# Kernel optimization log

Measured on AMD Instinct MI355X. Metric: run time of the kernel, lower is better.

The kernel has to match this reference:

```python
import math
import jax, jax.numpy as jnp
import numpy as np

B, L, H, E = 16, 2048, 8, 64
FACTOR = 1


def setup_inputs() -> dict:
    key = jax.random.key(0)
    kq, kk, kv = jax.random.split(key, 3)
    queries = jax.random.normal(kq, (B, L, H, E), dtype=jnp.float32)
    keys = jax.random.normal(kk, (B, L, H, E), dtype=jnp.float32)
    values = jax.random.normal(kv, (B, L, H, E), dtype=jnp.float32)
    return {"queries": queries, "keys": keys, "values": values, "attn_mask": 0}


def reference(queries, keys, values, attn_mask):
    # queries/keys/values: [B, L, H, E]; attn_mask is unused (as in the original).
    b, l, h, e = queries.shape
    # [B, H, E, L]
    qp = jnp.transpose(queries, (0, 2, 3, 1))
    kp = jnp.transpose(keys, (0, 2, 3, 1))
    vp = jnp.transpose(values, (0, 2, 3, 1))

    # Period-based dependency discovery via FFT cross-correlation.
    qf = jnp.fft.rfft(qp, axis=-1)
    kf = jnp.fft.rfft(kp, axis=-1)
    corr = jnp.fft.irfft(qf * jnp.conj(kf), n=l, axis=-1)  # [B, H, E, L]

    # Inference-style time-delay aggregation (per-batch top-k delays).
    top_k = max(1, int(FACTOR * math.log(l)))
    mean_value = corr.mean(axis=(1, 2))  # [B, L]
    weights, delay = jax.lax.top_k(mean_value, top_k)  # [B, K]
    tmp_corr = jax.nn.softmax(weights, axis=-1)  # [B, K]

    # Gather from doubled tensor == circular roll: index (t + delay) mod L.
    idx = (jnp.arange(l)[None, None, :] + delay[:, :, None]) % l  # [B, K, L]
    # vp[:, None]: [B, 1, H, E, L]; idx broadcast to [B, K, 1, 1, L]
    pattern = jnp.take_along_axis(vp[:, None], idx[:, :, None, None, :], axis=-1)  # [B, K, H, E, L]
    agg = jnp.einsum('bkhel,bk->bhel', pattern, tmp_corr)  # [B, H, E, L]

    return jnp.transpose(agg, (0, 3, 1, 2))  # [B, L, H, E]
```

## Files before the change

### kernel.cpp

```cpp
#include <hip/hip_runtime.h>
#include <hip/hip_fp16.h>
#include <cstdint>
#include <cstddef>

#define BB 16
#define LL 2048
#define CC 512
#define TK 7
#define PDC(a) ((a) + ((a) >> 4))
#define PSTR 1056
#define NG 128

typedef float2 cf;
typedef __attribute__((ext_vector_type(4))) float f32x4v;

__device__ inline cf cadd(cf a, cf b){ return make_float2(a.x + b.x, a.y + b.y); }
__device__ inline cf csub(cf a, cf b){ return make_float2(a.x - b.x, a.y - b.y); }
__device__ inline cf cmul(cf a, cf b){ return make_float2(a.x*b.x - a.y*b.y, a.x*b.y + a.y*b.x); }

template<int S> __device__ inline cf crot(cf z){
  return (S < 0) ? make_float2(z.y, -z.x) : make_float2(-z.y, z.x);
}

template<int S> __device__ inline void dft4(cf* x){
  const cf t0 = cadd(x[0], x[2]), t1 = csub(x[0], x[2]);
  const cf t2 = cadd(x[1], x[3]), t3 = csub(x[1], x[3]);
  const cf r = crot<S>(t3);
  x[0] = cadd(t0, t2); x[2] = csub(t0, t2);
  x[1] = cadd(t1, r);  x[3] = csub(t1, r);
}

template<int S> __device__ inline void dft8(cf* x){
  cf e[4] = { x[0], x[2], x[4], x[6] };
  cf o[4] = { x[1], x[3], x[5], x[7] };
  dft4<S>(e); dft4<S>(o);
  const float H = 0.70710678118654752440f;
  o[1] = cmul(o[1], make_float2(H, (float)S * H));
  o[2] = crot<S>(o[2]);
  o[3] = cmul(o[3], make_float2(-H, (float)S * H));
  x[0] = cadd(e[0], o[0]); x[4] = csub(e[0], o[0]);
  x[1] = cadd(e[1], o[1]); x[5] = csub(e[1], o[1]);
  x[2] = cadd(e[2], o[2]); x[6] = csub(e[2], o[2]);
  x[3] = cadd(e[3], o[3]); x[7] = csub(e[3], o[3]);
}

struct Tw { cf w2[7], w3[7], w4a[3], w4b[3]; };

template<int S>
__device__ inline void make_tw(int tid, Tw& T){
  const float base = (float)S * 6.283185307179586f / 2048.0f;
  const int j7 = tid & 7, j63 = tid & 63;
#pragma unroll
  for (int i = 0; i < 7; ++i){
    float s, c;
    __sincosf(base * (float)(32 * (i + 1) * j7), &s, &c);  T.w2[i] = make_float2(c, s);
    __sincosf(base * (float)( 4 * (i + 1) * j63), &s, &c); T.w3[i] = make_float2(c, s);
  }
#pragma unroll
  for (int i = 0; i < 3; ++i){
    float s, c;
    __sincosf(base * (float)((i + 1) * tid), &s, &c);         T.w4a[i] = make_float2(c, s);
    __sincosf(base * (float)((i + 1) * (tid + 256)), &s, &c); T.w4b[i] = make_float2(c, s);
  }
}

template<int S>
__device__ inline void fft_s123(cf* Bc, cf* Cc, cf* x, const Tw& T, int tid){
  dft8<S>(x);
#pragma unroll
  for (int t = 0; t < 8; ++t) Bc[PDC((tid << 3) + t)] = x[t];
  __syncthreads();
  {
    cf y[8];
#pragma unroll
    for (int t = 0; t < 8; ++t) y[t] = Bc[PDC(tid + (t << 8))];
#pragma unroll
    for (int t = 1; t < 8; ++t) y[t] = cmul(y[t], T.w2[t - 1]);
    dft8<S>(y);
    const int base = ((tid >> 3) << 6) + (tid & 7);
#pragma unroll
    for (int t = 0; t < 8; ++t) Cc[PDC(base + (t << 3))] = y[t];
  }
  __syncthreads();
  {
    cf y[8];
#pragma unroll
    for (int t = 0; t < 8; ++t) y[t] = Cc[PDC(tid + (t << 8))];
#pragma unroll
    for (int t = 1; t < 8; ++t) y[t] = cmul(y[t], T.w3[t - 1]);
    dft8<S>(y);
    const int base = ((tid >> 6) << 9) + (tid & 63);
#pragma unroll
    for (int t = 0; t < 8; ++t) Bc[PDC(base + (t << 6))] = y[t];
  }
  __syncthreads();
}

__global__ __launch_bounds__(256) void transpose_pack(const float* __restrict__ q,
                                                      const float* __restrict__ k,
                                                      __half2* __restrict__ z){
  int bid = blockIdx.x;
  const int tt = bid & 31; bid >>= 5;
  const int ct = bid & 7;  bid >>= 3;
  const int b = bid;
  const int t0 = tt << 6, c0 = ct << 6;
  __shared__ __half2 T[64][69];
  const int tid = threadIdx.x;
  const size_t inbase = ((size_t)b * LL + t0) * CC + c0;
  const int c4 = (tid & 15) << 2;
  f32x4v a[4], e[4];
#pragma unroll
  for (int p2 = 0; p2 < 4; ++p2){
    const int row = (p2 << 4) + (tid >> 4);
    a[p2] = __builtin_nontemporal_load(
        reinterpret_cast<const f32x4v*>(q + inbase + (size_t)row * CC + c4));
    e[p2] = __builtin_nontemporal_load(
        reinterpret_cast<const f32x4v*>(k + inbase + (size_t)row * CC + c4));
  }
#pragma unroll
  for (int p2 = 0; p2 < 4; ++p2){
    const int row = (p2 << 4) + (tid >> 4);
    T[row][c4 + 0] = __floats2half2_rn(a[p2][0], e[p2][0]);
    T[row][c4 + 1] = __floats2half2_rn(a[p2][1], e[p2][1]);
    T[row][c4 + 2] = __floats2half2_rn(a[p2][2], e[p2][2]);
    T[row][c4 + 3] = __floats2half2_rn(a[p2][3], e[p2][3]);
  }
  __syncthreads();
  const size_t outbase = ((size_t)b * CC + c0) * LL + (size_t)t0;
#pragma unroll
  for (int it = 0; it < 4; ++it){
    const int idx = (it << 8) + tid;
    const int c = idx >> 4;
    const int t4 = (idx & 15) << 2;
    const __half2 u0 = T[t4 + 0][c], u1 = T[t4 + 1][c];
    const __half2 u2 = T[t4 + 2][c], u3 = T[t4 + 3][c];
    uint4 w;
    w.x = *reinterpret_cast<const uint*>(&u0);
    w.y = *reinterpret_cast<const uint*>(&u1);
    w.z = *reinterpret_cast<const uint*>(&u2);
    w.w = *reinterpret_cast<const uint*>(&u3);
    *reinterpret_cast<uint4*>(&z[outbase + (size_t)c * LL + t4]) = w;
  }
}

__global__ __launch_bounds__(256) void fft_fwd(const __half2* __restrict__ z,
                                               float2* __restrict__ Ppart){
  int bid = blockIdx.x;
  const int g = bid & (NG - 1); const int b = bid >> 7;
  const int tid = threadIdx.x;
  __shared__ cf B[2176];
  Tw T; make_tw<-1>(tid, T);
  const __half2* zg = z + (((size_t)b * CC + (size_t)g * 4) << 11);
  float accRe[4] = {0,0,0,0};
  float accIm[4] = {0,0,0,0};
  float acc1024 = 0.f;
  __half2 h[8];
#pragma unroll
  for (int t = 0; t < 8; ++t) h[t] = zg[tid + (t << 8)];
  for (int ch = 0; ch < 4; ++ch){
    cf x[8];
#pragma unroll
    for (int t = 0; t < 8; ++t) x[t] = __half22float2(h[t]);
    if (ch < 3){
      const __half2* zn = zg + ((size_t)(ch + 1) << 11);
#pragma unroll
      for (int t = 0; t < 8; ++t) h[t] = zn[tid + (t << 8)];
    }
    dft8<-1>(x);
    __syncthreads();
#pragma unroll
    for (int t = 0; t < 8; ++t) B[PDC((tid << 3) + t)] = x[t];
    __syncthreads();
    cf y[8];
#pragma unroll
    for (int t = 0; t < 8; ++t) y[t] = B[PDC(tid + (t << 8))];
#pragma unroll
    for (int t = 1; t < 8; ++t) y[t] = cmul(y[t], T.w2[t - 1]);
    dft8<-1>(y);
    __syncthreads();
    {
      const int base = ((tid >> 3) << 6) + (tid & 7);
#pragma unroll
      for (int t = 0; t < 8; ++t) B[PDC(base + (t << 3))] = y[t];
    }
    __syncthreads();
#pragma unroll
    for (int t = 0; t < 8; ++t) y[t] = B[PDC(tid + (t << 8))];
#pragma unroll
    for (int t = 1; t < 8; ++t) y[t] = cmul(y[t], T.w3[t - 1]);
    dft8<-1>(y);
    __syncthreads();
    {
      const int base = ((tid >> 6) << 9) + (tid & 63);
#pragma unroll
      for (int t = 0; t < 8; ++t) B[PDC(base + (t << 6))] = y[t];
    }
    __syncthreads();
    cf y0[4], y1[4];
#pragma unroll
    for (int t = 0; t < 4; ++t) y0[t] = B[PDC(tid + (t << 9))];
#pragma unroll
    for (int t = 0; t < 4; ++t) y1[t] = B[PDC(tid + 256 + (t << 9))];
#pragma unroll
    for (int t = 1; t < 4; ++t){
      y0[t] = cmul(y0[t], T.w4a[t - 1]);
      y1[t] = cmul(y1[t], T.w4b[t - 1]);
    }
    dft4<-1>(y0); dft4<-1>(y1);
#pragma unroll
    for (int t = 0; t < 4; ++t) B[PDC(tid + (t << 9))] = y0[t];
#pragma unroll
    for (int t = 0; t < 4; ++t) B[PDC(tid + 256 + (t << 9))] = y1[t];
    __syncthreads();
    const cf Areg[4] = { y0[0], y1[0], y0[1], y1[1] };
#pragma unroll
    for (int r = 0; r < 4; ++r){
      const int f = tid + (r << 8);
      const int p = (2048 - f) & 2047;
      const cf A = Areg[r];
      const cf Bv = B[PDC(p)];
      accRe[r] += 0.5f  * (Bv.y * A.x + Bv.x * A.y);
      accIm[r] += 0.25f * (A.x * A.x + A.y * A.y - Bv.x * Bv.x - Bv.y * Bv.y);
    }
    if (tid == 0){
      const cf A = y0[2];
      acc1024 += A.x * A.y;
    }
  }
  float2* pp = Ppart + ((size_t)b * NG + g) * PSTR;
#pragma unroll
  for (int r = 0; r < 4; ++r)
    pp[tid + (r << 8)] = make_float2(accRe[r], accIm[r]);
  if (tid == 0) pp[1024] = make_float2(acc1024, 0.f);
}

__global__ __launch_bounds__(256) void reduce_P(const float2* __restrict__ Ppart,
                                                float2* __restrict__ P){
  const int gid = blockIdx.x * 256 + threadIdx.x;
  const int b = gid >> 11, f = gid & 2047;
  const int src = (f <= 1024) ? f : 2048 - f;
  const float sgn = (f <= 1024) ? 1.f : -1.f;
  float sr = 0.f, si = 0.f;
#pragma unroll 8
  for (int g = 0; g < NG; ++g){
    const float2 v = Ppart[((size_t)b * NG + g) * PSTR + src];
    sr += v.x; si += v.y;
  }
  P[((size_t)b << 11) + f] = make_float2(sr, sgn * si);
}

__global__ __launch_bounds__(256) void fft_inv_topk(const float2* __restrict__ P,
                                                    int* __restrict__ delays,
                                                    float* __restrict__ probs){
  const int b = blockIdx.x;
  const int tid = threadIdx.x;
  __shared__ cf Bc[2176];
  __shared__ cf Cc[2176];
  __shared__ float vals[2048];
  __shared__ float rv[256]; __shared__ int ri[256];
  __shared__ float wsel[TK]; __shared__ int dsel[TK];
  Tw T; make_tw<1>(tid, T);
  cf x[8];
#pragma unroll
  for (int t = 0; t < 8; ++t) x[t] = P[((size_t)b << 11) + tid + (t << 8)];
  fft_s123<1>(Bc, Cc, x, T, tid);
  const float scale = 1.0f / (2048.0f * 512.0f);
  {
#pragma unroll
    for (int hh = 0; hh < 2; ++hh){
      const int j = tid + (hh << 8);
      cf y[4];
#pragma unroll
      for (int t = 0; t < 4; ++t) y[t] = Bc[PDC(j + (t << 9))];
      const cf* w = hh ? T.w4b : T.w4a;
#pragma unroll
      for (int t = 1; t < 4; ++t) y[t] = cmul(y[t], w[t - 1]);
      dft4<1>(y);
#pragma unroll
      for (int t = 0; t < 4; ++t) vals[j + (t << 9)] = y[t].x * scale;
    }
  }
  __syncthreads();
  for (int kk = 0; kk < TK; ++kk){
    float best = -1e30f; int bi = LL;
    for (int i = tid; i < LL; i += 256){
      const float xv = vals[i];
      if (xv > best){ best = xv; bi = i; }
    }
    rv[tid] = best; ri[tid] = bi;
    __syncthreads();
    for (int s = 128; s > 0; s >>= 1){
      if (tid < s){
        const float ov = rv[tid + s]; const int oi = ri[tid + s];
        if (ov > rv[tid] || (ov == rv[tid] && oi < ri[tid])){ rv[tid] = ov; ri[tid] = oi; }
      }
      __syncthreads();
    }
    if (tid == 0){ wsel[kk] = rv[0]; dsel[kk] = ri[0]; vals[ri[0]] = -1e30f; }
    __syncthreads();
  }
  if (tid == 0){
    const float m = wsel[0];
    float e[TK], ssum = 0.f;
#pragma unroll
    for (int i = 0; i < TK; ++i){ e[i] = expf(wsel[i] - m); ssum += e[i]; }
    const float inv = 1.0f / ssum;
#pragma unroll
    for (int i = 0; i < TK; ++i){
      probs[b * TK + i] = e[i] * inv;
      delays[b * TK + i] = dsel[i];
    }
  }
}

__global__ __launch_bounds__(256) void agg_out(const float* __restrict__ v,
                                               const int* __restrict__ delays,
                                               const float* __restrict__ probs,
                                               float* __restrict__ out){
  const int bid = blockIdx.x;
  const int xcd = bid & 7;
  const int w = bid >> 3;
  const int b = (xcd << 1) + (w >> 9);
  const int local = w & 511;
  const int tid = threadIdx.x;
  const int t = (local << 2) + (tid >> 6);
  const int i0 = tid & 63;
  const int row = (b << 11) + t;
  float p[TK]; int d[TK];
#pragma unroll
  for (int kk = 0; kk < TK; ++kk){
    d[kk] = delays[b * TK + kk];
    p[kk] = probs[b * TK + kk];
  }
  const f32x4v* v4 = reinterpret_cast<const f32x4v*>(v);
  f32x4v x0[TK], x1[TK];
#pragma unroll
  for (int kk = 0; kk < TK; ++kk){
    const int srcr = (t + d[kk]) & (LL - 1);
    const size_t base = (size_t)((b << 11) + srcr) * 128;
    x0[kk] = v4[base + i0];
    x1[kk] = v4[base + i0 + 64];
  }
  f32x4v acc0 = {0.f, 0.f, 0.f, 0.f};
  f32x4v acc1 = {0.f, 0.f, 0.f, 0.f};
#pragma unroll
  for (int kk = 0; kk < TK; ++kk){
    acc0 += x0[kk] * p[kk];
    acc1 += x1[kk] * p[kk];
  }
  f32x4v* o = reinterpret_cast<f32x4v*>(out) + (size_t)row * 128;
  __builtin_nontemporal_store(acc0, o + i0);
  __builtin_nontemporal_store(acc1, o + i0 + 64);
}

extern "C" void kernel_launch(void* const* d_in, const int* in_sizes, int n_in,
                              void* d_out, int out_size, void* d_ws, size_t ws_size,
                              hipStream_t stream){
  const float* q = (const float*)d_in[0];
  const float* k = (const float*)d_in[1];
  const float* v = (const float*)d_in[2];
  float* out = (float*)d_out;

  char* ws = (char*)d_ws;
  const size_t Z_BYTES  = (size_t)BB * CC * LL * sizeof(__half2);
  const size_t PP_BYTES = (size_t)BB * NG * PSTR * sizeof(float2);
  const size_t P_BYTES  = (size_t)BB * LL * sizeof(float2);
  __half2* zbuf = (__half2*)ws;
  float2* Ppart = (float2*)(ws + Z_BYTES);
  float2* Pbuf  = (float2*)(ws + Z_BYTES + PP_BYTES);
  int* delays = (int*)(ws + Z_BYTES + PP_BYTES + P_BYTES);
  float* probs = (float*)(ws + Z_BYTES + PP_BYTES + P_BYTES + 1024);

  hipLaunchKernelGGL(transpose_pack, dim3(BB * 32 * 8), dim3(256), 0, stream, q, k, zbuf);
  hipLaunchKernelGGL(fft_fwd, dim3(BB * NG), dim3(256), 0, stream, zbuf, Ppart);
  hipLaunchKernelGGL(reduce_P, dim3((BB * LL) / 256), dim3(256), 0, stream, Ppart, Pbuf);
  hipLaunchKernelGGL(fft_inv_topk, dim3(BB), dim3(256), 0, stream, Pbuf, delays, probs);
  hipLaunchKernelGGL(agg_out, dim3(BB * 512), dim3(256), 0, stream,
                     v, delays, probs, out);
}
```

Measured before the change: 115.9 us.

## Make agg_out persistent with double-buffered gather loads across eight row iterations

After: 133.4 us. +15.1%, slower.

```diff
diff --git a/kernel.cpp b/kernel.cpp
--- a/kernel.cpp
+++ b/kernel.cpp
@@ -319,38 +319,55 @@
                                                float* __restrict__ out){
   const int bid = blockIdx.x;
   const int xcd = bid & 7;
-  const int w = bid >> 3;
-  const int b = (xcd << 1) + (w >> 9);
-  const int local = w & 511;
+  const int j0  = bid >> 3;
   const int tid = threadIdx.x;
-  const int t = (local << 2) + (tid >> 6);
-  const int i0 = tid & 63;
-  const int row = (b << 11) + t;
-  float p[TK]; int d[TK];
-#pragma unroll
-  for (int kk = 0; kk < TK; ++kk){
-    d[kk] = delays[b * TK + kk];
-    p[kk] = probs[b * TK + kk];
+  const int row_off = tid >> 7;
+  const int slot = tid & 127;
+  const int b0 = xcd << 1;
+  float p0[TK], p1[TK]; int d0[TK], d1[TK];
+#pragma unroll
+  for (int k = 0; k < TK; ++k){
+    p0[k] = probs[b0 * TK + k];        d0[k] = delays[b0 * TK + k];
+    p1[k] = probs[(b0 + 1) * TK + k];  d1[k] = delays[(b0 + 1) * TK + k];
   }
   const f32x4v* v4 = reinterpret_cast<const f32x4v*>(v);
-  f32x4v x0[TK], x1[TK];
-#pragma unroll
-  for (int kk = 0; kk < TK; ++kk){
-    const int srcr = (t + d[kk]) & (LL - 1);
-    const size_t base = (size_t)((b << 11) + srcr) * 128;
-    x0[kk] = v4[base + i0];
-    x1[kk] = v4[base + i0 + 64];
-  }
-  f32x4v acc0 = {0.f, 0.f, 0.f, 0.f};
-  f32x4v acc1 = {0.f, 0.f, 0.f, 0.f};
-#pragma unroll
-  for (int kk = 0; kk < TK; ++kk){
-    acc0 += x0[kk] * p[kk];
-    acc1 += x1[kk] * p[kk];
-  }
-  f32x4v* o = reinterpret_cast<f32x4v*>(out) + (size_t)row * 128;
-  __builtin_nontemporal_store(acc0, o + i0);
-  __builtin_nontemporal_store(acc1, o + i0 + 64);
+  f32x4v A[TK], Bv[TK];
+
+#define AGG_ISSUE(s, X)                                                       \
+  {                                                                           \
+    const int it_ = j0 + ((s) << 8);                                          \
+    const int seg_ = it_ >> 10;                                               \
+    const int b_ = b0 + seg_;                                                 \
+    const int t_ = ((it_ << 1) + row_off) & (LL - 1);                         \
+    _Pragma("unroll")                                                         \
+    for (int k = 0; k < TK; ++k){                                             \
+      const int dk_ = seg_ ? d1[k] : d0[k];                                   \
+      const int src_ = (t_ + dk_) & (LL - 1);                                 \
+      X[k] = v4[(((size_t)((b_ << 11) + src_)) << 7) + slot];                 \
+    }                                                                         \
+  }
+
+  AGG_ISSUE(0, A);
+#pragma unroll
+  for (int s = 0; s < 8; ++s){
+    if (s & 1){ if (s < 7) AGG_ISSUE(s + 1, A); }
+    else      { if (s < 7) AGG_ISSUE(s + 1, Bv); }
+    const int it = j0 + (s << 8);
+    const int seg = it >> 10;
+    const int b = b0 + seg;
+    const int t = ((it << 1) + row_off) & (LL - 1);
+    f32x4v acc = {0.f, 0.f, 0.f, 0.f};
+    if (s & 1){
+#pragma unroll
+      for (int k = 0; k < TK; ++k) acc += Bv[k] * (seg ? p1[k] : p0[k]);
+    } else {
+#pragma unroll
+      for (int k = 0; k < TK; ++k) acc += A[k] * (seg ? p1[k] : p0[k]);
+    }
+    f32x4v* o = reinterpret_cast<f32x4v*>(out) + (((size_t)((b << 11) + t)) << 7) + slot;
+    __builtin_nontemporal_store(acc, o);
+  }
+#undef AGG_ISSUE
 }
 
 extern "C" void kernel_launch(void* const* d_in, const int* in_sizes, int n_in,
@@ -375,6 +392,6 @@
   hipLaunchKernelGGL(fft_fwd, dim3(BB * NG), dim3(256), 0, stream, zbuf, Ppart);
   hipLaunchKernelGGL(reduce_P, dim3((BB * LL) / 256), dim3(256), 0, stream, Ppart, Pbuf);
   hipLaunchKernelGGL(fft_inv_topk, dim3(BB), dim3(256), 0, stream, Pbuf, delays, probs);
-  hipLaunchKernelGGL(agg_out, dim3(BB * 512), dim3(256), 0, stream,
+  hipLaunchKernelGGL(agg_out, dim3(2048), dim3(256), 0, stream,
                      v, delays, probs, out);
 }
```
